# Kernel optimization log

Hardware: AMD Instinct MI355X
Metric: run time of the kernel (lower is better)

The kernel has to match this reference:

```python
import jax, jax.numpy as jnp
import numpy as np
from jax import lax

B, C, L, G = 2048, 9605, 20, 50
ALPHA, ALPHA1, ALPHA2, ALPHA3, ALPHA_OTHER = 0.5, 0.05, 2.0, 10.0, 0.5
NEG_INF = jnp.float32(-1e30)


def setup_inputs() -> dict:
    k0, k1, k2, k3 = jax.random.split(jax.random.key(0), 4)
    x = jax.random.normal(k0, (B, C), jnp.float32)
    # sparse multi-label targets (~10 positives/row) so at most ~1 whitelist group is active,
    # matching the original code's assert len(gt_whitelist_index) == 1
    y = (jax.random.uniform(k1, (B, C)) < 0.001).astype(jnp.int32)
    y_neg = (jax.random.uniform(k2, (B, C)) < 0.001).astype(jnp.int32)
    # L disjoint whitelist groups of G classes each (from mapping_dict in the original)
    idx = jax.random.permutation(k3, C)[: L * G].reshape(L, G)
    group_mask = jnp.zeros((L, C), bool).at[jnp.arange(L)[:, None], idx].set(True)
    return {"x": x, "y": y, "y_neg": y_neg, "group_mask": group_mask}


def _rank_loss(x1, x2, margin):
    # our_rank_loss: sigmoid(alpha3*(x2-x1+margin)), scaled by alpha2 when positive
    d = x2 - x1 + margin
    s = jax.nn.sigmoid(ALPHA3 * d)
    return jnp.where(d > 0, ALPHA2 * s, s)


def reference(x, y, y_neg, group_mask):
    xs = jax.nn.sigmoid(x)  # [B, C]
    gmf = group_mask.astype(jnp.float32)  # [L, C]

    # per-row max score inside each whitelist group -> [B, L]
    # lax.map over the L (=20) groups keeps peak memory at one [B, C] temp per step
    group_max = lax.map(
        lambda m: jnp.max(jnp.where(m, xs, NEG_INF), axis=-1), group_mask
    ).T  # [B, L]

    # find_gt_whitelist: group k active iff sum(y[group_k]) > 0
    active = jnp.einsum("bc,lc->bl", y.astype(jnp.float32), gmf) > 0
    active_neg = jnp.einsum("bc,lc->bl", y_neg.astype(jnp.float32), gmf) > 0
    has_gt = jnp.any(active, axis=-1)  # [B]
    g = jnp.argmax(active, axis=-1)  # first active group (original asserts exactly one)

    # top_k_thres = max(11th largest sigmoid score, alpha_other) in both branches
    thres = jnp.maximum(lax.top_k(xs, 11)[0][:, 10], ALPHA_OTHER)  # [B]

    # max over union of all whitelist classes (wl_indices)
    union_max = jnp.max(jnp.where(jnp.any(group_mask, 0)[None, :], xs, NEG_INF), -1)

    gt_max = jnp.take_along_axis(group_max, g[:, None], axis=1)[:, 0]  # [B]
    # incorrect_max: max(0, max over groups != g); incorrect_neg: max(0, max over neg-active groups)
    excl = jnp.where(jnp.arange(L)[None, :] == g[:, None], NEG_INF, group_max)
    incorrect_max = jnp.maximum(jnp.max(excl, -1), 0.0)
    incorrect_neg = jnp.maximum(jnp.max(jnp.where(active_neg, group_max, 0.0), -1), 0.0)

    # branch A: no gt whitelist group active
    case_a = (1 - ALPHA) * _rank_loss(thres, union_max, ALPHA1) + ALPHA * _rank_loss(
        thres, incorrect_neg, ALPHA1
    )
    # branch B: exactly one gt group g
    case_b = (
        _rank_loss(gt_max, thres, ALPHA1)
        + jnp.where(
            incorrect_max > 0, (1 - ALPHA) * _rank_loss(thres, incorrect_max, ALPHA1), 0.0
        )
        + jnp.where(
            incorrect_neg > 0,
            ALPHA * _rank_loss(thres, incorrect_neg, ALPHA1),
            ALPHA * _rank_loss(thres, incorrect_max, ALPHA1),
        )
    )
    return jnp.sum(jnp.where(has_gt, case_b, case_a))
```

## Files before the change

kernel.cpp:

```cpp
#include <hip/hip_runtime.h>
#include <stdint.h>

#define B_ROWS 2048
#define C_CLS  9605
#define L_GRP  20
#define GM_BYTES (L_GRP * C_CLS)
#define REPSTRIDE 9728
#define GID_REGION (4 * REPSTRIDE)
#define NEG_BIG -3.0e38f

__device__ __forceinline__ float sigmoidf(float v) {
  return 1.0f / (1.0f + __expf(-v));
}

__device__ __forceinline__ float rank_loss(float x1, float x2) {
  float d = x2 - x1 + 0.05f;
  float s = 1.0f / (1.0f + __expf(-10.0f * d));
  return d > 0.0f ? 2.0f * s : s;
}

__device__ __forceinline__ unsigned fmap(float f) {
  unsigned u = __float_as_uint(f);
  return (u & 0x80000000u) ? ~u : (u | 0x80000000u);
}
__device__ __forceinline__ float funmap(unsigned m) {
  unsigned u = (m & 0x80000000u) ? (m ^ 0x80000000u) : ~m;
  return __uint_as_float(u);
}

__global__ void probe_init_kernel(const uint4* __restrict__ gm,
                                  unsigned char* __restrict__ ws,
                                  float* __restrict__ out,
                                  int* __restrict__ flag) {
  __shared__ int s_part[16];
  const int tid = threadIdx.x;
  if (tid == 0) out[0] = 0.0f;
  uint4* gfill = (uint4*)(ws + 64);
  const unsigned F = 0xFFFFFFFFu;
  for (int i = tid; i < GID_REGION / 16; i += 1024)
    gfill[i] = make_uint4(F, F, F, F);
  int local = 0;
  const int nvec = GM_BYTES / 16;
  for (int i = tid; i < nvec; i += 1024) {
    uint4 w = gm[i];
    unsigned a[4] = {w.x, w.y, w.z, w.w};
#pragma unroll
    for (int q = 0; q < 4; ++q) {
      local += ((a[q] & 0x000000FFu) != 0) + ((a[q] & 0x0000FF00u) != 0) +
               ((a[q] & 0x00FF0000u) != 0) + ((a[q] & 0xFF000000u) != 0);
    }
  }
  if (tid == 0) {
    const unsigned char* gb = (const unsigned char*)gm;
    for (int i = nvec * 16; i < GM_BYTES; ++i) local += (gb[i] != 0);
  }
#pragma unroll
  for (int off = 32; off; off >>= 1) local += __shfl_xor(local, off);
  if ((tid & 63) == 0) s_part[tid >> 6] = local;
  __syncthreads();
  if (tid == 0) {
    int tot = 0;
    for (int w = 0; w < 16; ++w) tot += s_part[w];
    *flag = tot;
  }
}

__global__ void build_gid_kernel(const void* gm, const int* __restrict__ flag,
                                 unsigned char* __restrict__ ws) {
  int i = blockIdx.x * blockDim.x + threadIdx.x;
  if (i >= GM_BYTES) return;
  const bool is_byte = (*flag > 600);
  bool m;
  if (is_byte) m = ((const unsigned char*)gm)[i] != 0;
  else         m = ((const unsigned int*)gm)[i] != 0u;
  if (m) {
    int l = i / C_CLS;
    int c = i - l * C_CLS;
    unsigned char* base = ws + 64;
#pragma unroll
    for (int r = 0; r < 4; ++r) base[r * REPSTRIDE + r + c] = (unsigned char)l;
  }
}

__global__ __launch_bounds__(256, 4) void loss_kernel(
    const float* __restrict__ x, const int* __restrict__ y,
    const int* __restrict__ yn, const unsigned char* __restrict__ ws64,
    float* __restrict__ out) {
  __shared__ unsigned s_gmax[L_GRP];
  __shared__ unsigned s_act, s_actn;
  __shared__ float s_wtop[4 * 11];
  const int tid = threadIdx.x;
  const int lane = tid & 63;
  const int wave = tid >> 6;
  const int row = blockIdx.x;

  const size_t base = (size_t)row * C_CLS;
  const int mis = (int)(base & 3);
  const int peel = (4 - mis) & 3;
  const float* xr = x + base;
  const int* yr = y + base;
  const int* nr = yn + base;
  const unsigned char* gidc = ws64 + mis * REPSTRIDE + mis;

  if (tid < L_GRP) s_gmax[tid] = 0u;
  if (tid == 0) { s_act = 0u; s_actn = 0u; }
  __syncthreads();

  float t[11];
#pragma unroll
  for (int i = 0; i < 11; ++i) t[i] = 0.0f;
  unsigned actL = 0u, actnL = 0u;

  auto ins = [&](float v) {
    if (v > t[10]) {
      float a = v;
#pragma unroll
      for (int i = 0; i < 11; ++i) {
        float hi = fmaxf(t[i], a); a = fminf(t[i], a); t[i] = hi;
      }
    }
  };
  auto gmax_upd = [&](unsigned gk, float v) {
    unsigned fm = fmap(v);
    if (fm > s_gmax[gk]) atomicMax(&s_gmax[gk], fm);
  };
  auto edge = [&](int c) {
    float v = xr[c];
    ins(v);
    unsigned gk = gidc[c];
    if (gk < L_GRP) {
      gmax_upd(gk, v);
      unsigned bit = 1u << gk;
      if (yr[c] != 0) actL |= bit;
      if (nr[c] != 0) actnL |= bit;
    }
  };

  if (tid < peel) edge(tid);
  const int nvec = (C_CLS - peel) >> 2;
  const int tail0 = peel + (nvec << 2);
  if (tid < C_CLS - tail0) edge(tail0 + tid);

  const float4* x4 = (const float4*)(xr + peel);
  const int4* y4 = (const int4*)(yr + peel);
  const int4* n4 = (const int4*)(nr + peel);
  const unsigned* g4 = (const unsigned*)(gidc + peel);

  auto quad = [&](float4 xv, int4 yv, int4 nv, unsigned gw) {
    if (gw != 0xFFFFFFFFu) {
      unsigned g0 = gw & 0xFFu, g1 = (gw >> 8) & 0xFFu,
               g2 = (gw >> 16) & 0xFFu, g3 = gw >> 24;
      if (g0 < L_GRP) gmax_upd(g0, xv.x);
      if (g1 < L_GRP) gmax_upd(g1, xv.y);
      if (g2 < L_GRP) gmax_upd(g2, xv.z);
      if (g3 < L_GRP) gmax_upd(g3, xv.w);
    }
    if (yv.x | yv.y | yv.z | yv.w | nv.x | nv.y | nv.z | nv.w) {
      const int yq[4] = {yv.x, yv.y, yv.z, yv.w};
      const int nq[4] = {nv.x, nv.y, nv.z, nv.w};
      const unsigned gq[4] = {gw & 0xFFu, (gw >> 8) & 0xFFu,
                              (gw >> 16) & 0xFFu, gw >> 24};
#pragma unroll
      for (int q = 0; q < 4; ++q) {
        if ((yq[q] | nq[q]) && gq[q] < L_GRP) {
          unsigned bit = 1u << gq[q];
          if (yq[q]) actL |= bit;
          if (nq[q]) actnL |= bit;
        }
      }
    }
    float am = fmaxf(fmaxf(xv.x, xv.y), fmaxf(xv.z, xv.w));
    if (am > t[10]) { ins(xv.x); ins(xv.y); ins(xv.z); ins(xv.w); }
  };

  int j = tid;
  for (; j + 768 < nvec; j += 1024) {
    float4 xa = x4[j];
    float4 xb = x4[j + 256];
    float4 xc = x4[j + 512];
    float4 xd = x4[j + 768];
    int4 ya = y4[j];
    int4 yb = y4[j + 256];
    int4 yc = y4[j + 512];
    int4 yd = y4[j + 768];
    int4 na = n4[j];
    int4 nb = n4[j + 256];
    int4 nc = n4[j + 512];
    int4 nd = n4[j + 768];
    unsigned ga = g4[j];
    unsigned gb = g4[j + 256];
    unsigned gc = g4[j + 512];
    unsigned gd = g4[j + 768];
    quad(xa, ya, na, ga);
    quad(xb, yb, nb, gb);
    quad(xc, yc, nc, gc);
    quad(xd, yd, nd, gd);
  }
  for (; j < nvec; j += 256) {
    quad(x4[j], y4[j], n4[j], g4[j]);
  }

  if (actL) atomicOr(&s_act, actL);
  if (actnL) atomicOr(&s_actn, actnL);

  float cur = t[0];
  float mr[11];
#pragma unroll
  for (int r = 0; r < 11; ++r) {
    float m = cur;
#pragma unroll
    for (int off = 32; off; off >>= 1) m = fmaxf(m, __shfl_xor(m, off));
    mr[r] = m;
    if (r < 10) {
      unsigned long long b = __ballot(cur == m);
      int leader = (int)(__ffsll(b) - 1);
      if (lane == leader) {
#pragma unroll
        for (int i = 0; i < 10; ++i) t[i] = t[i + 1];
        t[10] = NEG_BIG;
        cur = t[0];
      }
    }
  }
  if (lane == 0) {
#pragma unroll
    for (int r = 0; r < 11; ++r) s_wtop[wave * 11 + r] = mr[r];
  }
  __syncthreads();

  if (wave == 0) {
    float v = (lane < 44) ? s_wtop[lane] : NEG_BIG;
    float eleventh = NEG_BIG;
#pragma unroll
    for (int r = 0; r < 11; ++r) {
      float m = v;
#pragma unroll
      for (int off = 32; off; off >>= 1) m = fmaxf(m, __shfl_xor(m, off));
      eleventh = m;
      if (r < 10) {
        unsigned long long b = __ballot(v == m);
        int leader = (int)(__ffsll(b) - 1);
        if (lane == leader) v = NEG_BIG;
      }
    }

    const unsigned aL = s_act, anL = s_actn;
    const bool has_gt = (aL != 0u);
    const int g = has_gt ? (__ffs(aL) - 1) : 0;
    const float thres = fmaxf(sigmoidf(eleventh), 0.5f);

    float union_max = NEG_BIG, gt_sg = 0.0f, inc_max = NEG_BIG, inc_neg = 0.0f;
#pragma unroll
    for (int l = 0; l < L_GRP; ++l) {
      float sg = sigmoidf(funmap(s_gmax[l]));
      union_max = fmaxf(union_max, sg);
      if (l == g) gt_sg = sg; else inc_max = fmaxf(inc_max, sg);
      if ((anL >> l) & 1u) inc_neg = fmaxf(inc_neg, sg);
    }
    inc_max = fmaxf(inc_max, 0.0f);
    inc_neg = fmaxf(inc_neg, 0.0f);

    float loss;
    if (has_gt) {
      loss = rank_loss(gt_sg, thres);
      if (inc_max > 0.0f) loss += 0.5f * rank_loss(thres, inc_max);
      loss += 0.5f * rank_loss(thres, (inc_neg > 0.0f) ? inc_neg : inc_max);
    } else {
      loss = 0.5f * rank_loss(thres, union_max) + 0.5f * rank_loss(thres, inc_neg);
    }
    if (lane == 0) atomicAdd(out, loss);
  }
}

extern "C" void kernel_launch(void* const* d_in, const int* in_sizes, int n_in,
                              void* d_out, int out_size, void* d_ws, size_t ws_size,
                              hipStream_t stream) {
  (void)in_sizes; (void)n_in; (void)out_size; (void)ws_size;
  const float* x = (const float*)d_in[0];
  const int* y = (const int*)d_in[1];
  const int* yn = (const int*)d_in[2];
  const void* gm = d_in[3];

  int* flag = (int*)d_ws;
  unsigned char* ws = (unsigned char*)d_ws;
  unsigned char* ws64 = ws + 64;

  probe_init_kernel<<<1, 1024, 0, stream>>>((const uint4*)gm, ws,
                                            (float*)d_out, flag);
  build_gid_kernel<<<(GM_BYTES + 255) / 256, 256, 0, stream>>>(gm, flag, ws);
  loss_kernel<<<B_ROWS, 256, 0, stream>>>(x, y, yn, ws64, (float*)d_out);
}
```

Measured before the change: 255.1 us.

## Split loss kernel into separate label-activity and score-reduction kernels

Splits the single fused per-row kernel into two kernels. The first scans y and y_neg to compute per-row active-group bitmasks, written to workspace. The second scans x for the top-11 and the group maxima, reading those bitmasks. The aim is to lighten register and instruction pressure in each pass and raise occupancy for the label scan. In exchange it adds a kernel launch and a workspace round trip, and it gives up overlapping x loads with label loads.

```diff
diff --git a/kernel.cpp b/kernel.cpp
--- a/kernel.cpp
+++ b/kernel.cpp
@@ -7,6 +7,8 @@
 #define GM_BYTES (L_GRP * C_CLS)
 #define REPSTRIDE 9728
 #define GID_REGION (4 * REPSTRIDE)
+#define ACT_OFF (64 + GID_REGION)
+#define ACTN_OFF (ACT_OFF + 4 * B_ROWS)
 #define NEG_BIG -3.0e38f
 
 __device__ __forceinline__ float sigmoidf(float v) {
@@ -82,103 +84,55 @@
   }
 }
 
-__global__ __launch_bounds__(256, 4) void loss_kernel(
-    const float* __restrict__ x, const int* __restrict__ y,
-    const int* __restrict__ yn, const unsigned char* __restrict__ ws64,
-    float* __restrict__ out) {
-  __shared__ unsigned s_gmax[L_GRP];
+__global__ __launch_bounds__(256, 8) void act_kernel(
+    const int* __restrict__ y, const int* __restrict__ yn,
+    const unsigned char* __restrict__ ws64, int* __restrict__ act,
+    int* __restrict__ actn) {
   __shared__ unsigned s_act, s_actn;
-  __shared__ float s_wtop[4 * 11];
   const int tid = threadIdx.x;
-  const int lane = tid & 63;
-  const int wave = tid >> 6;
   const int row = blockIdx.x;
-
   const size_t base = (size_t)row * C_CLS;
-  const int mis = (int)(base & 3);
-  const int peel = (4 - mis) & 3;
-  const float* xr = x + base;
+  const int peel = (4 - (int)(base & 3)) & 3;
   const int* yr = y + base;
   const int* nr = yn + base;
-  const unsigned char* gidc = ws64 + mis * REPSTRIDE + mis;
-
-  if (tid < L_GRP) s_gmax[tid] = 0u;
+
   if (tid == 0) { s_act = 0u; s_actn = 0u; }
   __syncthreads();
 
-  float t[11];
-#pragma unroll
-  for (int i = 0; i < 11; ++i) t[i] = 0.0f;
   unsigned actL = 0u, actnL = 0u;
-
-  auto ins = [&](float v) {
-    if (v > t[10]) {
-      float a = v;
-#pragma unroll
-      for (int i = 0; i < 11; ++i) {
-        float hi = fmaxf(t[i], a); a = fminf(t[i], a); t[i] = hi;
+  auto mark = [&](int c, int yv, int nv) {
+    if (yv | nv) {
+      unsigned g = ws64[c];
+      if (g < L_GRP) {
+        unsigned bit = 1u << g;
+        if (yv) actL |= bit;
+        if (nv) actnL |= bit;
       }
     }
   };
-  auto gmax_upd = [&](unsigned gk, float v) {
-    unsigned fm = fmap(v);
-    if (fm > s_gmax[gk]) atomicMax(&s_gmax[gk], fm);
-  };
-  auto edge = [&](int c) {
-    float v = xr[c];
-    ins(v);
-    unsigned gk = gidc[c];
-    if (gk < L_GRP) {
-      gmax_upd(gk, v);
-      unsigned bit = 1u << gk;
-      if (yr[c] != 0) actL |= bit;
-      if (nr[c] != 0) actnL |= bit;
-    }
-  };
-
-  if (tid < peel) edge(tid);
+
+  if (tid < peel) mark(tid, yr[tid], nr[tid]);
   const int nvec = (C_CLS - peel) >> 2;
   const int tail0 = peel + (nvec << 2);
-  if (tid < C_CLS - tail0) edge(tail0 + tid);
-
-  const float4* x4 = (const float4*)(xr + peel);
+  if (tid < C_CLS - tail0) {
+    int c = tail0 + tid;
+    mark(c, yr[c], nr[c]);
+  }
+
   const int4* y4 = (const int4*)(yr + peel);
   const int4* n4 = (const int4*)(nr + peel);
-  const unsigned* g4 = (const unsigned*)(gidc + peel);
-
-  auto quad = [&](float4 xv, int4 yv, int4 nv, unsigned gw) {
-    if (gw != 0xFFFFFFFFu) {
-      unsigned g0 = gw & 0xFFu, g1 = (gw >> 8) & 0xFFu,
-               g2 = (gw >> 16) & 0xFFu, g3 = gw >> 24;
-      if (g0 < L_GRP) gmax_upd(g0, xv.x);
-      if (g1 < L_GRP) gmax_upd(g1, xv.y);
-      if (g2 < L_GRP) gmax_upd(g2, xv.z);
-      if (g3 < L_GRP) gmax_upd(g3, xv.w);
-    }
+
+  auto quad = [&](int4 yv, int4 nv, int c0) {
     if (yv.x | yv.y | yv.z | yv.w | nv.x | nv.y | nv.z | nv.w) {
-      const int yq[4] = {yv.x, yv.y, yv.z, yv.w};
-      const int nq[4] = {nv.x, nv.y, nv.z, nv.w};
-      const unsigned gq[4] = {gw & 0xFFu, (gw >> 8) & 0xFFu,
-                              (gw >> 16) & 0xFFu, gw >> 24};
-#pragma unroll
-      for (int q = 0; q < 4; ++q) {
-        if ((yq[q] | nq[q]) && gq[q] < L_GRP) {
-          unsigned bit = 1u << gq[q];
-          if (yq[q]) actL |= bit;
-          if (nq[q]) actnL |= bit;
-        }
-      }
-    }
-    float am = fmaxf(fmaxf(xv.x, xv.y), fmaxf(xv.z, xv.w));
-    if (am > t[10]) { ins(xv.x); ins(xv.y); ins(xv.z); ins(xv.w); }
+      mark(c0, yv.x, nv.x);
+      mark(c0 + 1, yv.y, nv.y);
+      mark(c0 + 2, yv.z, nv.z);
+      mark(c0 + 3, yv.w, nv.w);
+    }
   };
 
   int j = tid;
   for (; j + 768 < nvec; j += 1024) {
-    float4 xa = x4[j];
-    float4 xb = x4[j + 256];
-    float4 xc = x4[j + 512];
-    float4 xd = x4[j + 768];
     int4 ya = y4[j];
     int4 yb = y4[j + 256];
     int4 yc = y4[j + 512];
@@ -187,21 +141,103 @@
     int4 nb = n4[j + 256];
     int4 nc = n4[j + 512];
     int4 nd = n4[j + 768];
+    quad(ya, na, peel + 4 * j);
+    quad(yb, nb, peel + 4 * (j + 256));
+    quad(yc, nc, peel + 4 * (j + 512));
+    quad(yd, nd, peel + 4 * (j + 768));
+  }
+  for (; j < nvec; j += 256) quad(y4[j], n4[j], peel + 4 * j);
+
+  if (actL) atomicOr(&s_act, actL);
+  if (actnL) atomicOr(&s_actn, actnL);
+  __syncthreads();
+  if (tid == 0) {
+    act[row] = (int)s_act;
+    actn[row] = (int)s_actn;
+  }
+}
+
+__global__ __launch_bounds__(256, 4) void x_kernel(
+    const float* __restrict__ x, const unsigned char* __restrict__ ws64,
+    const int* __restrict__ act, const int* __restrict__ actn,
+    float* __restrict__ out) {
+  __shared__ unsigned s_gmax[L_GRP];
+  __shared__ float s_wtop[4 * 11];
+  const int tid = threadIdx.x;
+  const int lane = tid & 63;
+  const int wave = tid >> 6;
+  const int row = blockIdx.x;
+
+  const size_t base = (size_t)row * C_CLS;
+  const int mis = (int)(base & 3);
+  const int peel = (4 - mis) & 3;
+  const float* xr = x + base;
+  const unsigned char* gidc = ws64 + mis * REPSTRIDE + mis;
+
+  if (tid < L_GRP) s_gmax[tid] = 0u;
+  __syncthreads();
+
+  float t[11];
+#pragma unroll
+  for (int i = 0; i < 11; ++i) t[i] = 0.0f;
+
+  auto ins = [&](float v) {
+    if (v > t[10]) {
+      float a = v;
+#pragma unroll
+      for (int i = 0; i < 11; ++i) {
+        float hi = fmaxf(t[i], a); a = fminf(t[i], a); t[i] = hi;
+      }
+    }
+  };
+  auto gmax_upd = [&](unsigned gk, float v) {
+    unsigned fm = fmap(v);
+    if (fm > s_gmax[gk]) atomicMax(&s_gmax[gk], fm);
+  };
+  auto edge = [&](int c) {
+    float v = xr[c];
+    ins(v);
+    unsigned gk = gidc[c];
+    if (gk < L_GRP) gmax_upd(gk, v);
+  };
+
+  if (tid < peel) edge(tid);
+  const int nvec = (C_CLS - peel) >> 2;
+  const int tail0 = peel + (nvec << 2);
+  if (tid < C_CLS - tail0) edge(tail0 + tid);
+
+  const float4* x4 = (const float4*)(xr + peel);
+  const unsigned* g4 = (const unsigned*)(gidc + peel);
+
+  auto quad = [&](float4 xv, unsigned gw) {
+    if (gw != 0xFFFFFFFFu) {
+      unsigned g0 = gw & 0xFFu, g1 = (gw >> 8) & 0xFFu,
+               g2 = (gw >> 16) & 0xFFu, g3 = gw >> 24;
+      if (g0 < L_GRP) gmax_upd(g0, xv.x);
+      if (g1 < L_GRP) gmax_upd(g1, xv.y);
+      if (g2 < L_GRP) gmax_upd(g2, xv.z);
+      if (g3 < L_GRP) gmax_upd(g3, xv.w);
+    }
+    float am = fmaxf(fmaxf(xv.x, xv.y), fmaxf(xv.z, xv.w));
+    if (am > t[10]) { ins(xv.x); ins(xv.y); ins(xv.z); ins(xv.w); }
+  };
+
+  int j = tid;
+  for (; j + 768 < nvec; j += 1024) {
+    float4 xa = x4[j];
+    float4 xb = x4[j + 256];
+    float4 xc = x4[j + 512];
+    float4 xd = x4[j + 768];
     unsigned ga = g4[j];
     unsigned gb = g4[j + 256];
     unsigned gc = g4[j + 512];
     unsigned gd = g4[j + 768];
-    quad(xa, ya, na, ga);
-    quad(xb, yb, nb, gb);
-    quad(xc, yc, nc, gc);
-    quad(xd, yd, nd, gd);
-  }
-  for (; j < nvec; j += 256) {
-    quad(x4[j], y4[j], n4[j], g4[j]);
-  }
-
-  if (actL) atomicOr(&s_act, actL);
-  if (actnL) atomicOr(&s_actn, actnL);
+    quad(xa, ga);
+    quad(xb, gb);
+    quad(xc, gc);
+    quad(xd, gd);
+  }
+  for (; j < nvec; j += 256) quad(x4[j], g4[j]);
 
   float cur = t[0];
   float mr[11];
@@ -244,7 +280,8 @@
       }
     }
 
-    const unsigned aL = s_act, anL = s_actn;
+    const unsigned aL = (unsigned)act[row];
+    const unsigned anL = (unsigned)actn[row];
     const bool has_gt = (aL != 0u);
     const int g = has_gt ? (__ffs(aL) - 1) : 0;
     const float thres = fmaxf(sigmoidf(eleventh), 0.5f);
@@ -284,9 +321,12 @@
   int* flag = (int*)d_ws;
   unsigned char* ws = (unsigned char*)d_ws;
   unsigned char* ws64 = ws + 64;
+  int* act = (int*)(ws + ACT_OFF);
+  int* actn = (int*)(ws + ACTN_OFF);
 
   probe_init_kernel<<<1, 1024, 0, stream>>>((const uint4*)gm, ws,
                                             (float*)d_out, flag);
   build_gid_kernel<<<(GM_BYTES + 255) / 256, 256, 0, stream>>>(gm, flag, ws);
-  loss_kernel<<<B_ROWS, 256, 0, stream>>>(x, y, yn, ws64, (float*)d_out);
-}
+  act_kernel<<<B_ROWS, 256, 0, stream>>>(y, yn, ws64, act, actn);
+  x_kernel<<<B_ROWS, 256, 0, stream>>>(x, ws64, act, actn, (float*)d_out);
+}
```

Measured after the change: 273.4 us. 1.07x slower.

## Split y/y_neg activity scan into a flat grid-stride kernel

Applied to the files above, without the earlier changes.

Moves the scan of the sparse y and y_neg label arrays out of the per-row loss kernel into a separate flat grid-stride kernel. That kernel reads the labels as uint4 over the whole flattened array and atomically ORs group bits into per-row words in workspace. The loss kernel then only streams x and the group-id map, which lightens its per-row work, and its occupancy hint is raised. The cost is an extra kernel launch, global atomics, and a dependency between the two kernels, while the total bytes read stay the same.

```diff
diff --git a/kernel.cpp b/kernel.cpp
--- a/kernel.cpp
+++ b/kernel.cpp
@@ -7,7 +7,12 @@
 #define GM_BYTES (L_GRP * C_CLS)
 #define REPSTRIDE 9728
 #define GID_REGION (4 * REPSTRIDE)
+#define ACT_OFF (64 + GID_REGION)
+#define ACTN_OFF (ACT_OFF + 4 * B_ROWS)
 #define NEG_BIG -3.0e38f
+
+#define NELEM (B_ROWS * C_CLS)
+#define N4 (NELEM / 4)
 
 __device__ __forceinline__ float sigmoidf(float v) {
   return 1.0f / (1.0f + __expf(-v));
@@ -39,6 +44,8 @@
   const unsigned F = 0xFFFFFFFFu;
   for (int i = tid; i < GID_REGION / 16; i += 1024)
     gfill[i] = make_uint4(F, F, F, F);
+  unsigned* actz = (unsigned*)(ws + ACT_OFF);
+  for (int i = tid; i < 2 * B_ROWS; i += 1024) actz[i] = 0u;
   int local = 0;
   const int nvec = GM_BYTES / 16;
   for (int i = tid; i < nvec; i += 1024) {
@@ -82,12 +89,51 @@
   }
 }
 
-__global__ __launch_bounds__(256, 4) void loss_kernel(
-    const float* __restrict__ x, const int* __restrict__ y,
-    const int* __restrict__ yn, const unsigned char* __restrict__ ws64,
+__global__ __launch_bounds__(256, 8) void flat_act_kernel(
+    const uint4* __restrict__ yv4, const uint4* __restrict__ nv4,
+    const unsigned char* __restrict__ ws64, unsigned* __restrict__ act,
+    unsigned* __restrict__ actn) {
+  const int gs = gridDim.x * blockDim.x;
+  const int i0 = blockIdx.x * blockDim.x + threadIdx.x;
+
+  auto handle = [&](uint4 w, int i, unsigned* dst) {
+    if (w.x | w.y | w.z | w.w) {
+      const unsigned cq[4] = {w.x, w.y, w.z, w.w};
+#pragma unroll
+      for (int q = 0; q < 4; ++q) {
+        if (cq[q]) {
+          int e = 4 * i + q;
+          int r = e / C_CLS;
+          int c = e - r * C_CLS;
+          unsigned g = ws64[c];
+          if (g < L_GRP) atomicOr(&dst[r], 1u << g);
+        }
+      }
+    }
+  };
+  auto scan = [&](const uint4* __restrict__ p4, unsigned* __restrict__ dst) {
+    int i = i0;
+    for (; i + 3 * gs < N4; i += 4 * gs) {
+      uint4 a = p4[i];
+      uint4 b = p4[i + gs];
+      uint4 c = p4[i + 2 * gs];
+      uint4 d = p4[i + 3 * gs];
+      handle(a, i, dst);
+      handle(b, i + gs, dst);
+      handle(c, i + 2 * gs, dst);
+      handle(d, i + 3 * gs, dst);
+    }
+    for (; i < N4; i += gs) handle(p4[i], i, dst);
+  };
+  scan(yv4, act);
+  scan(nv4, actn);
+}
+
+__global__ __launch_bounds__(256, 8) void x_kernel(
+    const float* __restrict__ x, const unsigned char* __restrict__ ws64,
+    const unsigned* __restrict__ act, const unsigned* __restrict__ actn,
     float* __restrict__ out) {
   __shared__ unsigned s_gmax[L_GRP];
-  __shared__ unsigned s_act, s_actn;
   __shared__ float s_wtop[4 * 11];
   const int tid = threadIdx.x;
   const int lane = tid & 63;
@@ -98,18 +144,14 @@
   const int mis = (int)(base & 3);
   const int peel = (4 - mis) & 3;
   const float* xr = x + base;
-  const int* yr = y + base;
-  const int* nr = yn + base;
   const unsigned char* gidc = ws64 + mis * REPSTRIDE + mis;
 
   if (tid < L_GRP) s_gmax[tid] = 0u;
-  if (tid == 0) { s_act = 0u; s_actn = 0u; }
   __syncthreads();
 
   float t[11];
 #pragma unroll
   for (int i = 0; i < 11; ++i) t[i] = 0.0f;
-  unsigned actL = 0u, actnL = 0u;
 
   auto ins = [&](float v) {
     if (v > t[10]) {
@@ -128,12 +170,7 @@
     float v = xr[c];
     ins(v);
     unsigned gk = gidc[c];
-    if (gk < L_GRP) {
-      gmax_upd(gk, v);
-      unsigned bit = 1u << gk;
-      if (yr[c] != 0) actL |= bit;
-      if (nr[c] != 0) actnL |= bit;
-    }
+    if (gk < L_GRP) gmax_upd(gk, v);
   };
 
   if (tid < peel) edge(tid);
@@ -142,11 +179,9 @@
   if (tid < C_CLS - tail0) edge(tail0 + tid);
 
   const float4* x4 = (const float4*)(xr + peel);
-  const int4* y4 = (const int4*)(yr + peel);
-  const int4* n4 = (const int4*)(nr + peel);
   const unsigned* g4 = (const unsigned*)(gidc + peel);
 
-  auto quad = [&](float4 xv, int4 yv, int4 nv, unsigned gw) {
+  auto quad = [&](float4 xv, unsigned gw) {
     if (gw != 0xFFFFFFFFu) {
       unsigned g0 = gw & 0xFFu, g1 = (gw >> 8) & 0xFFu,
                g2 = (gw >> 16) & 0xFFu, g3 = gw >> 24;
@@ -155,20 +190,6 @@
       if (g2 < L_GRP) gmax_upd(g2, xv.z);
       if (g3 < L_GRP) gmax_upd(g3, xv.w);
     }
-    if (yv.x | yv.y | yv.z | yv.w | nv.x | nv.y | nv.z | nv.w) {
-      const int yq[4] = {yv.x, yv.y, yv.z, yv.w};
-      const int nq[4] = {nv.x, nv.y, nv.z, nv.w};
-      const unsigned gq[4] = {gw & 0xFFu, (gw >> 8) & 0xFFu,
-                              (gw >> 16) & 0xFFu, gw >> 24};
-#pragma unroll
-      for (int q = 0; q < 4; ++q) {
-        if ((yq[q] | nq[q]) && gq[q] < L_GRP) {
-          unsigned bit = 1u << gq[q];
-          if (yq[q]) actL |= bit;
-          if (nq[q]) actnL |= bit;
-        }
-      }
-    }
     float am = fmaxf(fmaxf(xv.x, xv.y), fmaxf(xv.z, xv.w));
     if (am > t[10]) { ins(xv.x); ins(xv.y); ins(xv.z); ins(xv.w); }
   };
@@ -179,29 +200,16 @@
     float4 xb = x4[j + 256];
     float4 xc = x4[j + 512];
     float4 xd = x4[j + 768];
-    int4 ya = y4[j];
-    int4 yb = y4[j + 256];
-    int4 yc = y4[j + 512];
-    int4 yd = y4[j + 768];
-    int4 na = n4[j];
-    int4 nb = n4[j + 256];
-    int4 nc = n4[j + 512];
-    int4 nd = n4[j + 768];
     unsigned ga = g4[j];
     unsigned gb = g4[j + 256];
     unsigned gc = g4[j + 512];
     unsigned gd = g4[j + 768];
-    quad(xa, ya, na, ga);
-    quad(xb, yb, nb, gb);
-    quad(xc, yc, nc, gc);
-    quad(xd, yd, nd, gd);
-  }
-  for (; j < nvec; j += 256) {
-    quad(x4[j], y4[j], n4[j], g4[j]);
-  }
-
-  if (actL) atomicOr(&s_act, actL);
-  if (actnL) atomicOr(&s_actn, actnL);
+    quad(xa, ga);
+    quad(xb, gb);
+    quad(xc, gc);
+    quad(xd, gd);
+  }
+  for (; j < nvec; j += 256) quad(x4[j], g4[j]);
 
   float cur = t[0];
   float mr[11];
@@ -244,7 +252,8 @@
       }
     }
 
-    const unsigned aL = s_act, anL = s_actn;
+    const unsigned aL = act[row];
+    const unsigned anL = actn[row];
     const bool has_gt = (aL != 0u);
     const int g = has_gt ? (__ffs(aL) - 1) : 0;
     const float thres = fmaxf(sigmoidf(eleventh), 0.5f);
@@ -284,9 +293,13 @@
   int* flag = (int*)d_ws;
   unsigned char* ws = (unsigned char*)d_ws;
   unsigned char* ws64 = ws + 64;
+  unsigned* act = (unsigned*)(ws + ACT_OFF);
+  unsigned* actn = (unsigned*)(ws + ACTN_OFF);
 
   probe_init_kernel<<<1, 1024, 0, stream>>>((const uint4*)gm, ws,
                                             (float*)d_out, flag);
   build_gid_kernel<<<(GM_BYTES + 255) / 256, 256, 0, stream>>>(gm, flag, ws);
-  loss_kernel<<<B_ROWS, 256, 0, stream>>>(x, y, yn, ws64, (float*)d_out);
-}
+  flat_act_kernel<<<2048, 256, 0, stream>>>((const uint4*)y, (const uint4*)yn,
+                                            ws64, act, actn);
+  x_kernel<<<B_ROWS, 256, 0, stream>>>(x, ws64, act, actn, (float*)d_out);
+}
```

Result: slower. 273.3 us (+7.2%).
